# Kernel optimization log

Measured on AMD Instinct MI355X. Metric: run time of the kernel, lower is better.

## Reference

```python
import jax, jax.numpy as jnp
import numpy as np

N, IN_F, OUT_F = 4096, 512, 20000
S, M, EPS = 64.0, 0.5, 1e-7  # arcface defaults


def setup_inputs() -> dict:
    key = jax.random.key(0)
    kx, kl, kw = jax.random.split(key, 3)
    x = jax.random.normal(kx, (N, IN_F), dtype=jnp.float32)
    labels = jax.random.randint(kl, (N,), 0, OUT_F, dtype=jnp.int64)
    # nn.Linear default init: U(-1/sqrt(in), 1/sqrt(in))
    bound = 1.0 / np.sqrt(IN_F)
    W = jax.random.uniform(kw, (OUT_F, IN_F), dtype=jnp.float32, minval=-bound, maxval=bound)
    return {"x": x, "labels": labels, "W": W}


def reference(x, labels, W):
    # NOTE: the original torch code's weight-normalization loop is a no-op
    # (it rebinds a local variable), so only x is L2-normalized, faithfully.
    xn = x / jnp.maximum(jnp.linalg.norm(x, axis=1, keepdims=True), 1e-12)
    wf = xn @ W.T  # [N, OUT_F]
    diag = wf[jnp.arange(wf.shape[0]), labels]  # [N]
    # arcface margin: s * cos(acos(clamp(cos)) + m)
    numerator = S * jnp.cos(jnp.arccos(jnp.clip(diag, -1.0 + EPS, 1.0 - EPS)) + M)
    # 'excl' sum-exp over all classes except the label column, without the
    # per-sample slicing loop: full row sum-exp minus the diagonal term.
    excl_sum = jnp.sum(jnp.exp(S * wf), axis=1) - jnp.exp(S * diag)
    denominator = jnp.exp(numerator) + excl_sum
    L = numerator - jnp.log(denominator)
    return (-jnp.mean(L), wf)
```

## Files before the change

kernel.cpp:

```cpp
#include <hip/hip_runtime.h>
#include <hip/hip_bf16.h>


typedef unsigned short ushort;
typedef __attribute__((ext_vector_type(8))) __bf16 bf16x8;
typedef __attribute__((ext_vector_type(4))) float f32x4;
typedef __attribute__((ext_vector_type(8))) ushort ushortx8;

#define N_ROWS 4096
#define IN_F   512
#define OUT_F  20000
#define S_SCALE 64.0f
#define MARGIN  0.5f
#define EPS_C   1e-7f

typedef const __attribute__((address_space(1))) void* gas_ptr;
typedef __attribute__((address_space(3))) void* las_ptr;

__device__ inline void gload16(const void* g, void* l) {
    __builtin_amdgcn_global_load_lds((gas_ptr)g, (las_ptr)l, 16, 0, 0);
}

__device__ inline void bfsplit(float v, ushort& h, ushort& l) {
    __hip_bfloat16 hb = __float2bfloat16(v);
    float hf = __bfloat162float(hb);
    __hip_bfloat16 lb = __float2bfloat16(v - hf);
    h = *(ushort*)&hb;
    l = *(ushort*)&lb;
}

__global__ void prep_x_kernel(const float* __restrict__ x,
                              ushort* __restrict__ xh) {
    const int w    = threadIdx.x >> 6;
    const int lane = threadIdx.x & 63;
    const int row  = blockIdx.x * 4 + w;
    const float4* xr4 = (const float4*)(x + (size_t)row * IN_F);
    float4 a = xr4[lane * 2];
    float4 b = xr4[lane * 2 + 1];
    float v[8] = {a.x, a.y, a.z, a.w, b.x, b.y, b.z, b.w};
    float ss = 0.f;
#pragma unroll
    for (int i = 0; i < 8; ++i) ss += v[i] * v[i];
#pragma unroll
    for (int d = 1; d < 64; d <<= 1) ss += __shfl_xor(ss, d, 64);
    const float inv = 1.0f / fmaxf(sqrtf(ss), 1e-12f);
    ushortx8 h;
#pragma unroll
    for (int i = 0; i < 8; ++i) {
        __hip_bfloat16 hb = __float2bfloat16(v[i] * inv);
        h[i] = *(ushort*)&hb;
    }
    *(ushortx8*)(xh + (size_t)row * IN_F + lane * 8) = h;
}

__global__ void prep_w_kernel(const float* __restrict__ W,
                              ushort* __restrict__ Wh, ushort* __restrict__ Wl) {
    const int total = OUT_F * IN_F / 4;
    for (int i = blockIdx.x * blockDim.x + threadIdx.x; i < total;
         i += gridDim.x * blockDim.x) {
        float4 v = ((const float4*)W)[i];
        ushort4 h, l;
        bfsplit(v.x, h.x, l.x);
        bfsplit(v.y, h.y, l.y);
        bfsplit(v.z, h.z, l.z);
        bfsplit(v.w, h.w, l.w);
        ((ushort4*)Wh)[i] = h;
        ((ushort4*)Wl)[i] = l;
    }
}

__global__ __launch_bounds__(256, 2) void gemm_kernel(
    const ushort* __restrict__ xh,
    const ushort* __restrict__ Wh, const ushort* __restrict__ Wl,
    float* __restrict__ wf, float* __restrict__ rowsum)
{
    __shared__ ushort lds[3 * 4096];

    const int t    = threadIdx.x;
    const int lane = t & 63;
    const int w    = t >> 6;
    const int wr   = w >> 1, wc = w & 1;
    const int brow = blockIdx.x * 128;
    const int bcol = blockIdx.y * 128;

    const int c0 = w * 2, c1 = w * 2 + 1;
    const int sr0 = c0 * 16 + (lane >> 2);
    const int sr1 = c1 * 16 + (lane >> 2);
    const int sc  = (lane & 3) * 8;

    const int rB0 = min(bcol + sr0, OUT_F - 1);
    const int rB1 = min(bcol + sr1, OUT_F - 1);

    const ushort* gAh0 = xh + (size_t)(brow + sr0) * IN_F + sc;
    const ushort* gAh1 = xh + (size_t)(brow + sr1) * IN_F + sc;
    const ushort* gBh0 = Wh + (size_t)rB0 * IN_F + sc;
    const ushort* gBh1 = Wh + (size_t)rB1 * IN_F + sc;
    const ushort* gBl0 = Wl + (size_t)rB0 * IN_F + sc;
    const ushort* gBl1 = Wl + (size_t)rB1 * IN_F + sc;

    ushort* dAh0 = lds +         c0 * 512;
    ushort* dAh1 = lds +         c1 * 512;
    ushort* dBh0 = lds +  4096 + c0 * 512;
    ushort* dBh1 = lds +  4096 + c1 * 512;
    ushort* dBl0 = lds +  8192 + c0 * 512;
    ushort* dBl1 = lds +  8192 + c1 * 512;

    f32x4 acc[4][4];
#pragma unroll
    for (int m = 0; m < 4; ++m)
#pragma unroll
        for (int n = 0; n < 4; ++n) acc[m][n] = (f32x4){0.f, 0.f, 0.f, 0.f};

    const int aoff = (wr * 64 + (lane & 15)) * 32 + (lane >> 4) * 8;
    const int boff = (wc * 64 + (lane & 15)) * 32 + (lane >> 4) * 8;

    for (int kt = 0; kt < IN_F / 32; ++kt) {
        const int kOff = kt * 32;
        __syncthreads();
        gload16(gAh0 + kOff, dAh0);
        gload16(gAh1 + kOff, dAh1);
        gload16(gBh0 + kOff, dBh0);
        gload16(gBh1 + kOff, dBh1);
        gload16(gBl0 + kOff, dBl0);
        gload16(gBl1 + kOff, dBl1);
        __syncthreads();

        bf16x8 ah[4], bh[4], bl[4];
#pragma unroll
        for (int m = 0; m < 4; ++m)
            ah[m] = *(const bf16x8*)(lds +        aoff + m * 512);
#pragma unroll
        for (int n = 0; n < 4; ++n) {
            bh[n] = *(const bf16x8*)(lds + 4096 + boff + n * 512);
            bl[n] = *(const bf16x8*)(lds + 8192 + boff + n * 512);
        }
#pragma unroll
        for (int m = 0; m < 4; ++m)
#pragma unroll
            for (int n = 0; n < 4; ++n) {
                acc[m][n] = __builtin_amdgcn_mfma_f32_16x16x32_bf16(ah[m], bh[n], acc[m][n], 0, 0, 0);
                acc[m][n] = __builtin_amdgcn_mfma_f32_16x16x32_bf16(ah[m], bl[n], acc[m][n], 0, 0, 0);
            }
    }

    const int rbase = brow + wr * 64 + ((lane >> 4) << 2);
    const int cbase = bcol + wc * 64 + (lane & 15);
#pragma unroll
    for (int m = 0; m < 4; ++m) {
#pragma unroll
        for (int j = 0; j < 4; ++j) {
            const int r = rbase + m * 16 + j;
            const size_t rowoff = (size_t)r * OUT_F;
            float psum = 0.0f;
#pragma unroll
            for (int n = 0; n < 4; ++n) {
                const int ccol = cbase + n * 16;
                const float v = acc[m][n][j];
                if (ccol < OUT_F) {
                    wf[rowoff + ccol] = v;
                    psum += expf(S_SCALE * v);
                }
            }
#pragma unroll
            for (int d = 1; d < 16; d <<= 1) psum += __shfl_xor(psum, d, 16);
            if ((lane & 15) == 0) atomicAdd(&rowsum[r], psum);
        }
    }
}

__global__ void loss_partial_kernel(const float* __restrict__ x,
                                    const float* __restrict__ W,
                                    const float* __restrict__ wf,
                                    const float* __restrict__ rowsum,
                                    const int* __restrict__ labels,
                                    float* __restrict__ partial) {
    __shared__ float red[4];
    const int wid  = threadIdx.x >> 6;
    const int lane = threadIdx.x & 63;
    const int r    = blockIdx.x * 4 + wid;
    const int lab  = labels[r];

    const float4* xr = (const float4*)(x + (size_t)r * IN_F);
    const float4* wr = (const float4*)(W + (size_t)lab * IN_F);
    float4 xa = xr[lane * 2], xb = xr[lane * 2 + 1];
    float4 wa = wr[lane * 2], wb = wr[lane * 2 + 1];
    float ss  = xa.x*xa.x + xa.y*xa.y + xa.z*xa.z + xa.w*xa.w
              + xb.x*xb.x + xb.y*xb.y + xb.z*xb.z + xb.w*xb.w;
    float dot = xa.x*wa.x + xa.y*wa.y + xa.z*wa.z + xa.w*wa.w
              + xb.x*wb.x + xb.y*wb.y + xb.z*wb.z + xb.w*wb.w;
#pragma unroll
    for (int d = 1; d < 64; d <<= 1) {
        ss  += __shfl_xor(ss, d, 64);
        dot += __shfl_xor(dot, d, 64);
    }
    if (lane == 0) {
        const float diag_ex = dot / fmaxf(sqrtf(ss), 1e-12f);
        const float diag_wf = wf[(size_t)r * OUT_F + lab];
        const float c = fminf(fmaxf(diag_ex, -1.0f + EPS_C), 1.0f - EPS_C);
        const float num = S_SCALE * cosf(acosf(c) + MARGIN);
        const float excl = rowsum[r] - expf(S_SCALE * diag_wf);
        red[wid] = num - logf(expf(num) + excl);
    }
    __syncthreads();
    if (threadIdx.x == 0)
        partial[blockIdx.x] = red[0] + red[1] + red[2] + red[3];
}

__global__ void loss_final_kernel(const float* __restrict__ partial,
                                  float* __restrict__ out) {
    __shared__ float red[4];
    const int t = threadIdx.x;
    float v = 0.f;
#pragma unroll
    for (int i = 0; i < 4; ++i) v += partial[t * 4 + i];
#pragma unroll
    for (int d = 1; d < 64; d <<= 1) v += __shfl_xor(v, d, 64);
    if ((t & 63) == 0) red[t >> 6] = v;
    __syncthreads();
    if (t == 0)
        out[0] = -(red[0] + red[1] + red[2] + red[3]) / (float)N_ROWS;
}

extern "C" void kernel_launch(void* const* d_in, const int* in_sizes, int n_in,
                              void* d_out, int out_size, void* d_ws, size_t ws_size,
                              hipStream_t stream) {
    const float* x      = (const float*)d_in[0];
    const int*   labels = (const int*)d_in[1];
    const float* W      = (const float*)d_in[2];
    float* out = (float*)d_out;
    float* wf  = out + 1;

    char* ws = (char*)d_ws;
    float*  rowsum  = (float*)ws;
    float*  partial = (float*)(ws + 16384);
    ushort* xh = (ushort*)(ws + 20480);
    ushort* Wh = xh + (size_t)N_ROWS * IN_F;
    ushort* Wl = Wh + (size_t)OUT_F * IN_F;

    hipMemsetAsync(rowsum, 0, N_ROWS * sizeof(float), stream);
    prep_x_kernel<<<N_ROWS / 4, 256, 0, stream>>>(x, xh);
    prep_w_kernel<<<2048, 256, 0, stream>>>(W, Wh, Wl);
    gemm_kernel<<<dim3(N_ROWS / 128, (OUT_F + 127) / 128), 256, 0, stream>>>(
        xh, Wh, Wl, wf, rowsum);
    loss_partial_kernel<<<N_ROWS / 4, 256, 0, stream>>>(x, W, wf, rowsum, labels, partial);
    loss_final_kernel<<<1, 256, 0, stream>>>(partial, out);
}
```

Measured before the change: 557.7 us.

## Double-buffer LDS tiles to overlap global loads with MFMA compute

Doubles the shared-memory staging area so the next K-slice's global-to-LDS loads are issued before the MFMA work on the current slice. This replaces the two barriers per iteration with a prologue load and a single barrier per iteration. The goal is to hide global load latency behind matrix compute. In exchange, LDS use per block doubles to 48KB, which could limit occupancy, and correctness relies on the barrier also waiting for the outstanding async LDS loads.

```diff
diff --git a/kernel.cpp b/kernel.cpp
--- a/kernel.cpp
+++ b/kernel.cpp
@@ -74,7 +74,7 @@
     const ushort* __restrict__ Wh, const ushort* __restrict__ Wl,
     float* __restrict__ wf, float* __restrict__ rowsum)
 {
-    __shared__ ushort lds[3 * 4096];
+    __shared__ ushort lds[2 * 3 * 4096];
 
     const int t    = threadIdx.x;
     const int lane = t & 63;
@@ -98,12 +98,9 @@
     const ushort* gBl0 = Wl + (size_t)rB0 * IN_F + sc;
     const ushort* gBl1 = Wl + (size_t)rB1 * IN_F + sc;
 
-    ushort* dAh0 = lds +         c0 * 512;
-    ushort* dAh1 = lds +         c1 * 512;
-    ushort* dBh0 = lds +  4096 + c0 * 512;
-    ushort* dBh1 = lds +  4096 + c1 * 512;
-    ushort* dBl0 = lds +  8192 + c0 * 512;
-    ushort* dBl1 = lds +  8192 + c1 * 512;
+    const int oAh0 =         c0 * 512, oAh1 =         c1 * 512;
+    const int oBh0 = 4096 + c0 * 512, oBh1 = 4096 + c1 * 512;
+    const int oBl0 = 8192 + c0 * 512, oBl1 = 8192 + c1 * 512;
 
     f32x4 acc[4][4];
 #pragma unroll
@@ -114,25 +111,33 @@
     const int aoff = (wr * 64 + (lane & 15)) * 32 + (lane >> 4) * 8;
     const int boff = (wc * 64 + (lane & 15)) * 32 + (lane >> 4) * 8;
 
+    {
+        ushort* b = lds;
+        gload16(gAh0, b + oAh0); gload16(gAh1, b + oAh1);
+        gload16(gBh0, b + oBh0); gload16(gBh1, b + oBh1);
+        gload16(gBl0, b + oBl0); gload16(gBl1, b + oBl1);
+    }
+    __syncthreads();
+
+    int cur = 0;
     for (int kt = 0; kt < IN_F / 32; ++kt) {
-        const int kOff = kt * 32;
-        __syncthreads();
-        gload16(gAh0 + kOff, dAh0);
-        gload16(gAh1 + kOff, dAh1);
-        gload16(gBh0 + kOff, dBh0);
-        gload16(gBh1 + kOff, dBh1);
-        gload16(gBl0 + kOff, dBl0);
-        gload16(gBl1 + kOff, dBl1);
-        __syncthreads();
-
+        if (kt + 1 < IN_F / 32) {
+            const int kOff = (kt + 1) * 32;
+            ushort* b = lds + (cur ^ 1) * 12288;
+            gload16(gAh0 + kOff, b + oAh0); gload16(gAh1 + kOff, b + oAh1);
+            gload16(gBh0 + kOff, b + oBh0); gload16(gBh1 + kOff, b + oBh1);
+            gload16(gBl0 + kOff, b + oBl0); gload16(gBl1 + kOff, b + oBl1);
+        }
+
+        const ushort* b = lds + cur * 12288;
         bf16x8 ah[4], bh[4], bl[4];
 #pragma unroll
         for (int m = 0; m < 4; ++m)
-            ah[m] = *(const bf16x8*)(lds +        aoff + m * 512);
+            ah[m] = *(const bf16x8*)(b +        aoff + m * 512);
 #pragma unroll
         for (int n = 0; n < 4; ++n) {
-            bh[n] = *(const bf16x8*)(lds + 4096 + boff + n * 512);
-            bl[n] = *(const bf16x8*)(lds + 8192 + boff + n * 512);
+            bh[n] = *(const bf16x8*)(b + 4096 + boff + n * 512);
+            bl[n] = *(const bf16x8*)(b + 8192 + boff + n * 512);
         }
 #pragma unroll
         for (int m = 0; m < 4; ++m)
@@ -141,6 +146,9 @@
                 acc[m][n] = __builtin_amdgcn_mfma_f32_16x16x32_bf16(ah[m], bh[n], acc[m][n], 0, 0, 0);
                 acc[m][n] = __builtin_amdgcn_mfma_f32_16x16x32_bf16(ah[m], bl[n], acc[m][n], 0, 0, 0);
             }
+
+        __syncthreads();
+        cur ^= 1;
     }
 
     const int rbase = brow + wr * 64 + ((lane >> 4) << 2);
```

After: 548.3 us. No clear change (-1.7%).
